# Kernel optimization log

Hardware: AMD Instinct MI355X
Metric: run time of the kernel (lower is better)

The kernel has to match this reference:

```python
import jax, jax.numpy as jnp
import numpy as np
from jax import lax

B, T, D, H, L, OUT = 4, 1024, 1024, 16, 6, 1024
DH = D // H


def _ln(x, g, b, eps=1e-5):
    mu = jnp.mean(x, axis=-1, keepdims=True)
    var = jnp.mean(jnp.square(x - mu), axis=-1, keepdims=True)
    return (x - mu) * lax.rsqrt(var + eps) * g + b


def setup_inputs() -> dict:
    key = jax.random.key(0)
    ks = iter(jax.random.split(key, 32))
    s = 0.02
    inp = {
        "seq": jax.random.normal(next(ks), (B, T, D), jnp.float32),
        "pos_emb": jax.random.normal(next(ks), (1, T, D), jnp.float32) * s,
        # per-layer params stacked on leading L axis; linear weights stored [in, out]
        "ln1_g": jnp.ones((L, D), jnp.float32),
        "ln1_b": jnp.zeros((L, D), jnp.float32),
        "wq": jax.random.normal(next(ks), (L, D, D), jnp.float32) * s,
        "bq": jnp.zeros((L, D), jnp.float32),
        "wk": jax.random.normal(next(ks), (L, D, D), jnp.float32) * s,
        "bk": jnp.zeros((L, D), jnp.float32),
        "wv": jax.random.normal(next(ks), (L, D, D), jnp.float32) * s,
        "bv": jnp.zeros((L, D), jnp.float32),
        "wo": jax.random.normal(next(ks), (L, D, D), jnp.float32) * s,
        "bo": jnp.zeros((L, D), jnp.float32),
        "ln2_g": jnp.ones((L, D), jnp.float32),
        "ln2_b": jnp.zeros((L, D), jnp.float32),
        "w1": jax.random.normal(next(ks), (L, D, 4 * D), jnp.float32) * s,
        "b1": jnp.zeros((L, 4 * D), jnp.float32),
        "w2": jax.random.normal(next(ks), (L, 4 * D, D), jnp.float32) * s,
        "b2": jnp.zeros((L, D), jnp.float32),
        "lnf_g": jnp.ones((D,), jnp.float32),
        "lnf_b": jnp.zeros((D,), jnp.float32),
        "w_head": jax.random.normal(next(ks), (D, OUT), jnp.float32) * s,
    }
    return inp


def _gpt(seq, pos_emb, ln1_g, ln1_b, wq, bq, wk, bk, wv, bv, wo, bo,
         ln2_g, ln2_b, w1, b1, w2, b2, lnf_g, lnf_b, w_head):
    x = seq + pos_emb  # embedding dropout is identity in eval

    def block(x, p):
        (g1, b1g, Wq, Bq, Wk, Bk, Wv, Bv, Wo, Bo, g2, b2g, W1, B1, W2, B2) = p
        h = _ln(x, g1, b1g)
        q = (h @ Wq + Bq).reshape(B, T, H, DH)
        k = (h @ Wk + Bk).reshape(B, T, H, DH)
        v = (h @ Wv + Bv).reshape(B, T, H, DH)
        # NOTE: original mask buffer is all ones -> no causal masking (faithful)
        att = jnp.einsum('bthd,bshd->bhts', q, k) * (1.0 / np.sqrt(DH))
        att = jax.nn.softmax(att, axis=-1)
        y = jnp.einsum('bhts,bshd->bthd', att, v).reshape(B, T, D)
        x = x + (y @ Wo + Bo)
        h2 = _ln(x, g2, b2g)
        x = x + (jax.nn.gelu(h2 @ W1 + B1, approximate=False) @ W2 + B2)
        return x, None

    params = (ln1_g, ln1_b, wq, bq, wk, bk, wv, bv, wo, bo,
              ln2_g, ln2_b, w1, b1, w2, b2)
    x, _ = lax.scan(block, x, params)
    x = _ln(x, lnf_g, lnf_b)
    return x @ w_head


def reference(seq, pos_emb, ln1_g, ln1_b, wq, bq, wk, bk, wv, bv, wo, bo,
              ln2_g, ln2_b, w1, b1, w2, b2, lnf_g, lnf_b, w_head):
    return _gpt(seq, pos_emb, ln1_g, ln1_b, wq, bq, wk, bk, wv, bv, wo, bo,
                ln2_g, ln2_b, w1, b1, w2, b2, lnf_g, lnf_b, w_head)
```

## Files before the change

### kernel.cpp

```cpp
#include <hip/hip_runtime.h>
#include <math.h>

#define BB 4
#define TT 1024
#define DD 1024
#define HH 16
#define LL 6
#define DHH 64
#define MM (BB*TT)
#define QKVLD 3072

typedef short bf16x8 __attribute__((ext_vector_type(8)));
typedef float floatx4 __attribute__((ext_vector_type(4)));

__device__ __forceinline__ unsigned short f2bf(float f) {
    unsigned u = __builtin_bit_cast(unsigned, f);
    u += 0x7fffu + ((u >> 16) & 1u);
    return (unsigned short)(u >> 16);
}

__device__ __forceinline__ void glds16(const unsigned short* g, unsigned short* l) {
    __builtin_amdgcn_global_load_lds(
        (const __attribute__((address_space(1))) void*)g,
        (__attribute__((address_space(3))) void*)l, 16, 0, 0);
}

__global__ __launch_bounds__(256) void add_pos_kernel(
    const float* __restrict__ seq, const float* __restrict__ pos, float* __restrict__ x)
{
    int i = blockIdx.x * 256 + threadIdx.x;
    const int TD4 = TT * DD / 4;
    float4 s = ((const float4*)seq)[i];
    float4 p = ((const float4*)pos)[i & (TD4 - 1)];
    ((float4*)x)[i] = make_float4(s.x + p.x, s.y + p.y, s.z + p.z, s.w + p.w);
}

__global__ __launch_bounds__(256) void concat_bias_kernel(
    const float* __restrict__ bq, const float* __restrict__ bk,
    const float* __restrict__ bv, float* __restrict__ bqkv)
{
    int i = blockIdx.x * 256 + threadIdx.x;
    int l = i / QKVLD, j = i - l * QKVLD;
    float v;
    if (j < DD)            v = bq[l*DD + j];
    else if (j < 2*DD)     v = bk[l*DD + j - DD];
    else                   v = bv[l*DD + j - 2*DD];
    bqkv[i] = v;
}

__global__ __launch_bounds__(256) void ln_kernel(
    const float* __restrict__ x, const float* __restrict__ g,
    const float* __restrict__ b, unsigned short* __restrict__ out)
{
    __shared__ float red[8];
    int row = blockIdx.x;
    int tid = threadIdx.x;
    const float4* xr = (const float4*)(x + (size_t)row * DD);
    float4 v = xr[tid];
    float s  = v.x + v.y + v.z + v.w;
    float ss = v.x*v.x + v.y*v.y + v.z*v.z + v.w*v.w;
    #pragma unroll
    for (int o = 32; o > 0; o >>= 1) {
        s  += __shfl_down(s,  o, 64);
        ss += __shfl_down(ss, o, 64);
    }
    int wid = tid >> 6, lid = tid & 63;
    if (lid == 0) { red[wid] = s; red[4 + wid] = ss; }
    __syncthreads();
    float sum  = red[0] + red[1] + red[2] + red[3];
    float sums = red[4] + red[5] + red[6] + red[7];
    float mean = sum * (1.0f / DD);
    float var  = sums * (1.0f / DD) - mean * mean;
    float inv  = rsqrtf(var + 1e-5f);
    float4 gg = ((const float4*)g)[tid];
    float4 bb = ((const float4*)b)[tid];
    ushort4 o4;
    o4.x = f2bf((v.x - mean) * inv * gg.x + bb.x);
    o4.y = f2bf((v.y - mean) * inv * gg.y + bb.y);
    o4.z = f2bf((v.z - mean) * inv * gg.z + bb.z);
    o4.w = f2bf((v.w - mean) * inv * gg.w + bb.w);
    ((ushort4*)(out + (size_t)row * DD))[tid] = o4;
}

__global__ __launch_bounds__(256) void transpose_layer(
    const float* __restrict__ wq, const float* __restrict__ wk,
    const float* __restrict__ wv, const float* __restrict__ wo,
    const float* __restrict__ w1, const float* __restrict__ w2,
    unsigned short* __restrict__ wt)
{
    __shared__ float tile[32][33];
    const size_t DD2 = (size_t)DD * DD;
    int bid = blockIdx.x;
    const float* src; unsigned short* dst; int K, N, n0, k0;
    if (bid < 4096) {
        int r = bid >> 10, t = bid & 1023;
        src = (r == 0) ? wq : (r == 1) ? wk : (r == 2) ? wv : wo;
        dst = wt + (size_t)r * DD2; K = DD; N = DD;
        n0 = (t & 31) * 32; k0 = (t >> 5) * 32;
    } else if (bid < 8192) {
        int t = bid - 4096;
        src = w1; dst = wt + 4 * DD2; K = DD; N = 4 * DD;
        n0 = (t & 127) * 32; k0 = (t >> 7) * 32;
    } else {
        int t = bid - 8192;
        src = w2; dst = wt + 8 * DD2; K = 4 * DD; N = DD;
        n0 = (t & 31) * 32; k0 = (t >> 5) * 32;
    }
    int tx = threadIdx.x & 31, ty = threadIdx.x >> 5;
    #pragma unroll
    for (int i = 0; i < 4; i++)
        tile[ty + i*8][tx] = src[(size_t)(k0 + ty + i*8) * N + n0 + tx];
    __syncthreads();
    #pragma unroll
    for (int i = 0; i < 4; i++)
        dst[(size_t)(n0 + ty + i*8) * K + k0 + tx] = f2bf(tile[tx][ty + i*8]);
}

__global__ __launch_bounds__(256) void transpose_bf16(
    const float* __restrict__ W, unsigned short* __restrict__ Wt, int K, int N)
{
    __shared__ float tile[32][33];
    int n0 = blockIdx.x * 32, k0 = blockIdx.y * 32;
    int tx = threadIdx.x & 31, ty = threadIdx.x >> 5;
    #pragma unroll
    for (int i = 0; i < 4; i++)
        tile[ty + i*8][tx] = W[(size_t)(k0 + ty + i*8) * N + n0 + tx];
    __syncthreads();
    #pragma unroll
    for (int i = 0; i < 4; i++)
        Wt[(size_t)(n0 + ty + i*8) * K + k0 + tx] = f2bf(tile[tx][ty + i*8]);
}

template<int ACT, int RES, int OUTBF>
__global__ __launch_bounds__(256) void mfma_gemm(
    const unsigned short* __restrict__ A, const unsigned short* __restrict__ Bt,
    const float* __restrict__ bias, const float* __restrict__ res,
    void* __restrict__ Cv, int M, int N, int K)
{
    __shared__ unsigned short As[2][128*32];
    __shared__ unsigned short Bs[2][128*32];
    const int tid = threadIdx.x;
    const int wave = tid >> 6, lane = tid & 63;
    const int quad = lane >> 4, lc = lane & 15;

    const int bid = blockIdx.x;
    const int xcd = bid & 7;
    const int j = bid >> 3;
    const int m0 = (xcd * 4 + (j & 3)) << 7;
    const int n0 = (j >> 2) << 7;

    const int grow = wave * 32 + (lane >> 2);
    const int gcol = (lane & 3) * 8;
    const unsigned short* Ag = A  + (size_t)(m0 + grow) * K + gcol;
    const unsigned short* Bg = Bt + (size_t)(n0 + grow) * K + gcol;
    const int lbase = wave * 1024;

    const int wm = (wave & 1) * 64, wn = (wave >> 1) * 64;

    floatx4 acc[4][4];
    #pragma unroll
    for (int i = 0; i < 4; i++)
        #pragma unroll
        for (int jj = 0; jj < 4; jj++) acc[i][jj] = (floatx4)0.0f;

    glds16(Ag,                  &As[0][lbase]);
    glds16(Ag + (size_t)16 * K, &As[0][lbase + 512]);
    glds16(Bg,                  &Bs[0][lbase]);
    glds16(Bg + (size_t)16 * K, &Bs[0][lbase + 512]);
    __syncthreads();

    int cur = 0;
    for (int k0 = 0; k0 < K; k0 += 32) {
        if (k0 + 32 < K) {
            glds16(Ag + k0 + 32,                  &As[cur^1][lbase]);
            glds16(Ag + k0 + 32 + (size_t)16 * K, &As[cur^1][lbase + 512]);
            glds16(Bg + k0 + 32,                  &Bs[cur^1][lbase]);
            glds16(Bg + k0 + 32 + (size_t)16 * K, &Bs[cur^1][lbase + 512]);
        }
        bf16x8 af[4], bfr[4];
        #pragma unroll
        for (int i = 0; i < 4; i++)
            af[i] = *(const bf16x8*)&As[cur][(wm + i*16 + lc)*32 + quad*8];
        #pragma unroll
        for (int jj = 0; jj < 4; jj++)
            bfr[jj] = *(const bf16x8*)&Bs[cur][(wn + jj*16 + lc)*32 + quad*8];
        #pragma unroll
        for (int i = 0; i < 4; i++)
            #pragma unroll
            for (int jj = 0; jj < 4; jj++)
                acc[i][jj] = __builtin_amdgcn_mfma_f32_16x16x32_bf16(af[i], bfr[jj], acc[i][jj], 0, 0, 0);
        __syncthreads();
        cur ^= 1;
    }

    #pragma unroll
    for (int jj = 0; jj < 4; jj++) {
        int n = n0 + wn + jj*16 + lc;
        float bv = bias ? bias[n] : 0.0f;
        #pragma unroll
        for (int i = 0; i < 4; i++) {
            int mbase = m0 + wm + i*16 + quad*4;
            #pragma unroll
            for (int r = 0; r < 4; r++) {
                int m = mbase + r;
                float v = acc[i][jj][r] + bv;
                if (ACT) v = 0.5f * v * (1.0f + erff(v * 0.70710678118654752f));
                if (RES) v += res[(size_t)m * N + n];
                if (OUTBF) ((unsigned short*)Cv)[(size_t)m * N + n] = f2bf(v);
                else       ((float*)Cv)[(size_t)m * N + n] = v;
            }
        }
    }
}

#define LSTR 88
__global__ __launch_bounds__(256) void attn_mfma(
    const unsigned short* __restrict__ qkv, unsigned short* __restrict__ y)
{
    __shared__ unsigned short Qs[64*LSTR];
    __shared__ unsigned short Ks[64*LSTR];
    __shared__ unsigned short Ps[64*LSTR];
    const int tid = threadIdx.x, wave = tid >> 6, lane = tid & 63;
    const int quad = lane >> 4, lc = lane & 15;
    const int t0 = blockIdx.x * 64;
    const int b = blockIdx.y >> 4, h = blockIdx.y & 15;

    const unsigned short* q = qkv;
    const unsigned short* k = qkv + DD;
    const unsigned short* v = qkv + 2*DD;

    const size_t rowbase = (size_t)b * TT;
    const int sr = tid >> 2, sc = (tid & 3) * 16;

    {
        const unsigned short* src = q + (rowbase + t0 + sr) * QKVLD + h*DHH + sc;
        *(uint4*)&Qs[sr*LSTR + sc]     = *(const uint4*)src;
        *(uint4*)&Qs[sr*LSTR + sc + 8] = *(const uint4*)(src + 8);
    }

    float m_r[4], l_r[4];
    floatx4 o_acc[4];
    #pragma unroll
    for (int r = 0; r < 4; r++) { m_r[r] = -1e30f; l_r[r] = 0.0f; }
    #pragma unroll
    for (int f = 0; f < 4; f++) o_acc[f] = (floatx4)0.0f;

    for (int s0 = 0; s0 < TT; s0 += 64) {
        __syncthreads();
        {
            const unsigned short* src = k + (rowbase + s0 + sr) * QKVLD + h*DHH + sc;
            *(uint4*)&Ks[sr*LSTR + sc]     = *(const uint4*)src;
            *(uint4*)&Ks[sr*LSTR + sc + 8] = *(const uint4*)(src + 8);
        }
        __syncthreads();

        floatx4 s[4];
        #pragma unroll
        for (int f = 0; f < 4; f++) s[f] = (floatx4)0.0f;
        #pragma unroll
        for (int c = 0; c < 2; c++) {
            bf16x8 aq = *(const bf16x8*)&Qs[(wave*16 + lc)*LSTR + c*32 + quad*8];
            #pragma unroll
            for (int f = 0; f < 4; f++) {
                bf16x8 bk = *(const bf16x8*)&Ks[(f*16 + lc)*LSTR + c*32 + quad*8];
                s[f] = __builtin_amdgcn_mfma_f32_16x16x32_bf16(aq, bk, s[f], 0, 0, 0);
            }
        }

        #pragma unroll
        for (int r = 0; r < 4; r++) {
            float mt = fmaxf(fmaxf(s[0][r], s[1][r]), fmaxf(s[2][r], s[3][r])) * 0.125f;
            #pragma unroll
            for (int d = 1; d < 16; d <<= 1) mt = fmaxf(mt, __shfl_xor(mt, d, 64));
            float mn = fmaxf(m_r[r], mt);
            float alpha = __expf(m_r[r] - mn);
            m_r[r] = mn;
            float rs = 0.0f;
            #pragma unroll
            for (int f = 0; f < 4; f++) {
                float p = __expf(s[f][r] * 0.125f - mn);
                s[f][r] = p;
                rs += p;
            }
            #pragma unroll
            for (int d = 1; d < 16; d <<= 1) rs += __shfl_xor(rs, d, 64);
            l_r[r] = l_r[r] * alpha + rs;
            #pragma unroll
            for (int f = 0; f < 4; f++) o_acc[f][r] *= alpha;
        }

        #pragma unroll
        for (int f = 0; f < 4; f++)
            #pragma unroll
            for (int r = 0; r < 4; r++)
                Ps[(wave*16 + quad*4 + r)*LSTR + f*16 + lc] = f2bf(s[f][r]);

        __syncthreads();
        {
            const unsigned short* src = v + (rowbase + s0 + sr) * QKVLD + h*DHH + sc;
            uint4 v0 = *(const uint4*)src;
            uint4 v1 = *(const uint4*)(src + 8);
            unsigned short tmp[16];
            *(uint4*)&tmp[0] = v0;
            *(uint4*)&tmp[8] = v1;
            #pragma unroll
            for (int e = 0; e < 16; e++)
                Ks[(sc + e)*LSTR + sr] = tmp[e];
        }
        __syncthreads();

        #pragma unroll
        for (int c = 0; c < 2; c++) {
            bf16x8 ap = *(const bf16x8*)&Ps[(wave*16 + lc)*LSTR + c*32 + quad*8];
            #pragma unroll
            for (int f = 0; f < 4; f++) {
                bf16x8 bv = *(const bf16x8*)&Ks[(f*16 + lc)*LSTR + c*32 + quad*8];
                o_acc[f] = __builtin_amdgcn_mfma_f32_16x16x32_bf16(ap, bv, o_acc[f], 0, 0, 0);
            }
        }
    }

    unsigned short* yg = y + (rowbase + t0) * DD + h*DHH;
    #pragma unroll
    for (int f = 0; f < 4; f++)
        #pragma unroll
        for (int r = 0; r < 4; r++)
            yg[(size_t)(wave*16 + quad*4 + r) * DD + f*16 + lc] = f2bf(o_acc[f][r] / l_r[r]);
}

extern "C" void kernel_launch(void* const* d_in, const int* in_sizes, int n_in,
                              void* d_out, int out_size, void* d_ws, size_t ws_size,
                              hipStream_t stream)
{
    const float* seq    = (const float*)d_in[0];
    const float* pos    = (const float*)d_in[1];
    const float* ln1_g  = (const float*)d_in[2];
    const float* ln1_b  = (const float*)d_in[3];
    const float* wq     = (const float*)d_in[4];
    const float* bq     = (const float*)d_in[5];
    const float* wk     = (const float*)d_in[6];
    const float* bk     = (const float*)d_in[7];
    const float* wv     = (const float*)d_in[8];
    const float* bv     = (const float*)d_in[9];
    const float* wo     = (const float*)d_in[10];
    const float* bo     = (const float*)d_in[11];
    const float* ln2_g  = (const float*)d_in[12];
    const float* ln2_b  = (const float*)d_in[13];
    const float* w1     = (const float*)d_in[14];
    const float* b1     = (const float*)d_in[15];
    const float* w2     = (const float*)d_in[16];
    const float* b2     = (const float*)d_in[17];
    const float* lnf_g  = (const float*)d_in[18];
    const float* lnf_b  = (const float*)d_in[19];
    const float* w_head = (const float*)d_in[20];
    float* out = (float*)d_out;

    const size_t MSZ = (size_t)MM * DD;
    float* x            = (float*)d_ws;
    unsigned short* h   = (unsigned short*)(x + MSZ);
    unsigned short* qkv = h + MSZ;
    unsigned short* ub  = qkv + (size_t)MM * QKVLD;
    unsigned short* wt  = ub + (size_t)MM * 4 * DD;
    unsigned short* wto = wt + (size_t)3*DD*DD;
    unsigned short* wt1 = wt + (size_t)4*DD*DD;
    unsigned short* wt2 = wt + (size_t)8*DD*DD;
    float* bqkv         = (float*)(wt + (size_t)12*DD*DD);

    dim3 blk(256);
    dim3 g1(32*8);
    dim3 gq(32*24);
    dim3 g4(32*32);
    dim3 tsq(32, 32);
    dim3 ag(16, 64);

    add_pos_kernel<<<4096, blk, 0, stream>>>(seq, pos, x);
    concat_bias_kernel<<<LL*QKVLD/256, blk, 0, stream>>>(bq, bk, bv, bqkv);

    for (int l = 0; l < LL; l++) {
        const size_t wofs  = (size_t)l * DD * DD;
        const size_t bofs  = (size_t)l * DD;
        const size_t w1ofs = (size_t)l * DD * 4 * DD;
        const size_t b1ofs = (size_t)l * 4 * DD;

        transpose_layer<<<12288, blk, 0, stream>>>(
            wq + wofs, wk + wofs, wv + wofs, wo + wofs, w1 + w1ofs, w2 + w1ofs, wt);

        ln_kernel<<<MM, blk, 0, stream>>>(x, ln1_g + bofs, ln1_b + bofs, h);
        mfma_gemm<0,0,1><<<gq, blk, 0, stream>>>(h, wt, bqkv + (size_t)l*QKVLD, nullptr, qkv, MM, QKVLD, DD);
        attn_mfma<<<ag, blk, 0, stream>>>(qkv, h);
        mfma_gemm<0,1,0><<<g1, blk, 0, stream>>>(h, wto, bo + bofs, x, x, MM, DD, DD);
        ln_kernel<<<MM, blk, 0, stream>>>(x, ln2_g + bofs, ln2_b + bofs, h);
        mfma_gemm<1,0,1><<<g4, blk, 0, stream>>>(h, wt1, b1 + b1ofs, nullptr, ub, MM, 4*DD, DD);
        mfma_gemm<0,1,0><<<g1, blk, 0, stream>>>(ub, wt2, b2 + bofs, x, x, MM, DD, 4*DD);
    }

    ln_kernel<<<MM, blk, 0, stream>>>(x, lnf_g, lnf_b, h);
    transpose_bf16<<<tsq, blk, 0, stream>>>(w_head, wt, DD, DD);
    mfma_gemm<0,0,0><<<g1, blk, 0, stream>>>(h, wt, nullptr, nullptr, out, MM, DD, DD);
}
```

Measured before the change: 2.164 ms.

## Triple-buffer GEMM LDS tiles with partial vmcnt waits and one barrier per step

Turns the double-buffered direct-to-LDS load pipeline in the bf16 MFMA GEMM into a three-stage ring. Each step waits only for the oldest tile's loads (vmcnt(4)) before the barrier, so loads stay in flight across two k-steps. The end-of-iteration __syncthreads is removed. This adds LDS use (48KB), which may lower occupancy, and depends on hand-written waitcnt counts and a barrier-based WAR ordering being correct.

Result: no change. 2.170 ms (+0.3%).

```diff
diff --git a/kernel.cpp b/kernel.cpp
--- a/kernel.cpp
+++ b/kernel.cpp
@@ -137,8 +137,8 @@
     const float* __restrict__ bias, const float* __restrict__ res,
     void* __restrict__ Cv, int M, int N, int K)
 {
-    __shared__ unsigned short As[2][128*32];
-    __shared__ unsigned short Bs[2][128*32];
+    __shared__ unsigned short As[3][128*32];
+    __shared__ unsigned short Bs[3][128*32];
     const int tid = threadIdx.x;
     const int wave = tid >> 6, lane = tid & 63;
     const int quad = lane >> 4, lc = lane & 15;
@@ -163,19 +163,26 @@
         #pragma unroll
         for (int jj = 0; jj < 4; jj++) acc[i][jj] = (floatx4)0.0f;
 
-    glds16(Ag,                  &As[0][lbase]);
-    glds16(Ag + (size_t)16 * K, &As[0][lbase + 512]);
-    glds16(Bg,                  &Bs[0][lbase]);
-    glds16(Bg + (size_t)16 * K, &Bs[0][lbase + 512]);
-    __syncthreads();
+    #define STAGE(buf, koff) do { \
+        glds16(Ag + (koff),                 &As[buf][lbase]); \
+        glds16(Ag + (koff) + (size_t)16*K,  &As[buf][lbase + 512]); \
+        glds16(Bg + (koff),                 &Bs[buf][lbase]); \
+        glds16(Bg + (koff) + (size_t)16*K,  &Bs[buf][lbase + 512]); \
+    } while (0)
+
+    const int NT = K >> 5;
+    STAGE(0, 0);
+    STAGE(1, 32);
 
     int cur = 0;
-    for (int k0 = 0; k0 < K; k0 += 32) {
-        if (k0 + 32 < K) {
-            glds16(Ag + k0 + 32,                  &As[cur^1][lbase]);
-            glds16(Ag + k0 + 32 + (size_t)16 * K, &As[cur^1][lbase + 512]);
-            glds16(Bg + k0 + 32,                  &Bs[cur^1][lbase]);
-            glds16(Bg + k0 + 32 + (size_t)16 * K, &Bs[cur^1][lbase + 512]);
+    for (int t = 0, k0 = 0; t < NT; ++t, k0 += 32) {
+        if (t + 1 < NT) asm volatile("s_waitcnt vmcnt(4)" ::: "memory");
+        else            asm volatile("s_waitcnt vmcnt(0)" ::: "memory");
+        __builtin_amdgcn_s_barrier();
+        __builtin_amdgcn_sched_barrier(0);
+        if (t + 2 < NT) {
+            int nb = cur + 2; if (nb >= 3) nb -= 3;
+            STAGE(nb, k0 + 64);
         }
         bf16x8 af[4], bfr[4];
         #pragma unroll
@@ -189,9 +196,9 @@
             #pragma unroll
             for (int jj = 0; jj < 4; jj++)
                 acc[i][jj] = __builtin_amdgcn_mfma_f32_16x16x32_bf16(af[i], bfr[jj], acc[i][jj], 0, 0, 0);
-        __syncthreads();
-        cur ^= 1;
-    }
+        cur = (cur == 2) ? 0 : cur + 1;
+    }
+    #undef STAGE
 
     #pragma unroll
     for (int jj = 0; jj < 4; jj++) {
```
